# Kernel optimization log

Measured on AMD Instinct MI355X. Metric: run time of the kernel, lower is better.

The kernel has to match this reference:

```python
import jax, jax.numpy as jnp
import numpy as np

N_NODES = 100000
N_EDGES = 1600000
F_IN = 128
HIDDEN = 64
N_CLASSES = 32


def setup_inputs() -> dict:
    key = jax.random.key(0)
    k1, k2, k3, k4 = jax.random.split(key, 4)
    x = jax.random.normal(k1, (N_NODES, F_IN), dtype=jnp.float32)
    edge_index = jax.random.randint(k2, (2, N_EDGES), 0, N_NODES, dtype=jnp.int32)
    # Glorot-style init for the two GCNConv weight matrices
    W1 = jax.random.normal(k3, (F_IN, HIDDEN), dtype=jnp.float32) * (1.0 / np.sqrt(F_IN))
    W2 = jax.random.normal(k4, (HIDDEN, N_CLASSES), dtype=jnp.float32) * (1.0 / np.sqrt(HIDDEN))
    b1 = jnp.zeros((HIDDEN,), dtype=jnp.float32)
    b2 = jnp.zeros((N_CLASSES,), dtype=jnp.float32)
    return {"x": x, "edge_index": edge_index, "W1": W1, "b1": b1, "W2": W2, "b2": b2}


def gcn_conv(x, W, b, src, dst, num_nodes):
    # PyG GCNConv: linear transform first, then normalized neighbor aggregation.
    h = x @ W  # [N, out]
    ones = jnp.ones(src.shape, dtype=h.dtype)
    deg = jax.ops.segment_sum(ones, dst, num_segments=num_nodes)  # in-degree incl. self-loops
    d_inv_sqrt = jnp.where(deg > 0, jax.lax.rsqrt(deg), 0.0)
    norm = d_inv_sqrt[src] * d_inv_sqrt[dst]  # [E]
    msg = h[src] * norm[:, None]              # gather + scale, [E, out]
    out = jax.ops.segment_sum(msg, dst, num_segments=num_nodes)  # scatter-add
    return out + b


def reference(x, edge_index, W1, b1, W2, b2):
    n = x.shape[0]
    # add_self_loops=True (GCNConv default)
    loop = jnp.arange(n, dtype=edge_index.dtype)
    src = jnp.concatenate([edge_index[0], loop])
    dst = jnp.concatenate([edge_index[1], loop])
    h = jax.nn.relu(gcn_conv(x, W1, b1, src, dst, n))
    # F.dropout(training=self.training) is identity in eval mode
    logits = gcn_conv(h, W2, b2, src, dst, n)
    return jax.nn.log_softmax(logits, axis=1)
```

## Files before the change

### kernel.cpp

```cpp
#include <hip/hip_runtime.h>

#define F_IN 128
#define HID 64
#define CLS 32
#define BCAP 8192

typedef short v8s __attribute__((ext_vector_type(8)));
typedef float f4 __attribute__((ext_vector_type(4)));
typedef float f2 __attribute__((ext_vector_type(2)));

__device__ __forceinline__ float bflo(unsigned int w) { return __uint_as_float(w << 16); }
__device__ __forceinline__ float bfhi(unsigned int w) { return __uint_as_float(w & 0xFFFF0000u); }
__device__ __forceinline__ unsigned short f2bf(float f) {
    unsigned int u = __float_as_uint(f);
    u += 0x7FFFu + ((u >> 16) & 1u);
    return (unsigned short)(u >> 16);
}
__device__ __forceinline__ unsigned int pack2(float lo, float hi) {
    return (unsigned int)f2bf(lo) | ((unsigned int)f2bf(hi) << 16);
}
__device__ __forceinline__ unsigned char f2fp8(float v) {
    return (unsigned char)(__builtin_amdgcn_cvt_pk_fp8_f32(v, v, 0, false) & 0xFF);
}

__global__ __launch_bounds__(512) void k_init(int* __restrict__ bCursor, int nb) {
    int i = threadIdx.x;
    if (i < nb) bCursor[i] = i * BCAP;
}

__global__ __launch_bounds__(256) void k_bscatter(const int* __restrict__ src,
                                                  const int* __restrict__ dst,
                                                  int* __restrict__ bCursor,
                                                  int* __restrict__ bucketed, int E, int nb) {
    __shared__ int h[512];
    __shared__ int chunk[512];
    int tid = threadIdx.x;
    for (int i = tid; i < nb; i += 256) h[i] = 0;
    __syncthreads();

    int e0 = blockIdx.x * 2048;
    int myRec[8], myB[8], myRank[8];
#pragma unroll
    for (int k = 0; k < 8; ++k) {
        int e = e0 + k * 256 + tid;
        if (e < E) {
            int d = dst[e];
            myB[k] = d >> 8;
            myRec[k] = src[e] | ((d & 255) << 17);
            myRank[k] = atomicAdd(&h[myB[k]], 1);
        } else {
            myB[k] = -1;
        }
    }
    __syncthreads();
    for (int i = tid; i < nb; i += 256)
        chunk[i] = h[i] ? atomicAdd(&bCursor[i], h[i]) : 0;
    __syncthreads();
#pragma unroll
    for (int k = 0; k < 8; ++k) {
        if (myB[k] >= 0) bucketed[chunk[myB[k]] + myRank[k]] = myRec[k];
    }
}

__global__ __launch_bounds__(512) void k_csr(const int* __restrict__ bCursor,
                                             const int* __restrict__ bucketed,
                                             int* __restrict__ pk,
                                             float* __restrict__ dinv, int* __restrict__ csr,
                                             int n) {
    __shared__ int cnt[256];
    __shared__ int s[256];
    __shared__ int baseS[256];
    int b = blockIdx.x;
    int node0 = b << 8;
    int tid = threadIdx.x;
    if (tid < 256) cnt[tid] = 0;
    __syncthreads();
    int p0 = b * BCAP, p1 = bCursor[b];

    int rec[16], rnk[16];
#pragma unroll
    for (int k = 0; k < 16; ++k) {
        int p = p0 + tid + (k << 9);
        if (p < p1) {
            int r = bucketed[p];
            rec[k] = r;
            rnk[k] = atomicAdd(&cnt[r >> 17], 1);
        } else {
            rec[k] = -1;
        }
    }
    __syncthreads();
    int v = 0;
    if (tid < 256) { v = cnt[tid]; s[tid] = v; }
    __syncthreads();
    for (int off = 1; off < 256; off <<= 1) {
        int t = (tid >= off && tid < 256) ? s[tid - off] : 0;
        __syncthreads();
        if (tid < 256) s[tid] += t;
        __syncthreads();
    }
    if (tid < 256) {
        int myoff = p0 + s[tid] - v;
        baseS[tid] = myoff;
        int node = node0 + tid;
        if (node < n) {
            pk[node] = myoff | (v << 22);
            dinv[node] = rsqrtf((float)(v + 1));
        }
    }
    __syncthreads();
#pragma unroll
    for (int k = 0; k < 16; ++k) {
        if (rec[k] >= 0) csr[baseS[rec[k] >> 17] + rnk[k]] = rec[k] & 0x1FFFF;
    }
}

__global__ __launch_bounds__(256) void k_gemm1(const float* __restrict__ x,
                                               const float* __restrict__ W,
                                               const float* __restrict__ dinv,
                                               unsigned char* __restrict__ y, int n) {
    __shared__ unsigned short Wt[HID * 136];
    int tid = threadIdx.x;
    for (int i = tid; i < F_IN * HID; i += 256) {
        int k = i >> 6, nn = i & 63;
        Wt[nn * 136 + k] = f2bf(W[i]);
    }
    __syncthreads();

    int lane = tid & 63;
    int quad = lane >> 4, c = lane & 15;
    int nstripes = (n + 15) >> 4;
    int stripe = blockIdx.x * 4 + (tid >> 6);
    if (stripe >= nstripes) return;
    int row0 = stripe << 4;

    f4 acc[4] = {};
    union { unsigned int u[4]; v8s v; } au;

#pragma unroll
    for (int ks = 0; ks < 4; ++ks) {
        int k0 = ks * 32 + quad * 8;
        int row = row0 + c;
        if (row >= n) row = n - 1;
        const float* xp = x + (size_t)row * F_IN + k0;
        float4 lo = *(const float4*)xp;
        float4 hi = *(const float4*)(xp + 4);
        au.u[0] = pack2(lo.x, lo.y);
        au.u[1] = pack2(lo.z, lo.w);
        au.u[2] = pack2(hi.x, hi.y);
        au.u[3] = pack2(hi.z, hi.w);
        v8s a = au.v;
#pragma unroll
        for (int nt = 0; nt < 4; ++nt) {
            v8s bb = *(const v8s*)&Wt[(nt * 16 + c) * 136 + k0];
            acc[nt] = __builtin_amdgcn_mfma_f32_16x16x32_bf16(a, bb, acc[nt], 0, 0, 0);
        }
    }

#pragma unroll
    for (int reg = 0; reg < 4; ++reg) {
        int row = row0 + quad * 4 + reg;
        if (row < n) {
            float dd = dinv[row];
#pragma unroll
            for (int nt = 0; nt < 4; ++nt)
                y[(size_t)row * HID + nt * 16 + c] = f2fp8(acc[nt][reg] * dd);
        }
    }
}

__global__ __launch_bounds__(256) void k_gather64_w2(const int* __restrict__ pk,
                                                     const int* __restrict__ csr,
                                                     const unsigned char* __restrict__ xw8,
                                                     const float* __restrict__ b1,
                                                     const float* __restrict__ W2,
                                                     const float* __restrict__ dinv,
                                                     unsigned short* __restrict__ y2, int n) {
    __shared__ unsigned short Wt[CLS * 72];
    __shared__ unsigned short Hl[32 * 72];
    int tid = threadIdx.x;
    for (int i = tid; i < HID * CLS; i += 256) {
        int k = i >> 5, nn = i & 31;
        Wt[nn * 72 + k] = f2bf(W2[i]);
    }

    int g = tid >> 3;
    int l = tid & 7;
    int node = blockIdx.x * 32 + g;
    bool alive = node < n;

    if (alive) {
        unsigned int pv = (unsigned int)pk[node];
        int p0 = pv & 0x3FFFFF;
        int cntv = (int)(pv >> 22);
        int p1 = p0 + cntv;
        float dd = rsqrtf((float)(cntv + 1));
        uint2 sw = *(const uint2*)(xw8 + (size_t)node * HID + l * 8);

        f2 a0 = {0.f, 0.f}, a1 = a0, a2 = a0, a3 = a0;
        f2 c0 = a0, c1 = a0, c2 = a0, c3 = a0;
        int p = p0;
        for (; p + 3 < p1; p += 4) {
            int s0 = csr[p], s1 = csr[p + 1], s2 = csr[p + 2], s3 = csr[p + 3];
            uint2 w0 = *(const uint2*)(xw8 + (size_t)s0 * HID + l * 8);
            uint2 w1 = *(const uint2*)(xw8 + (size_t)s1 * HID + l * 8);
            uint2 w2 = *(const uint2*)(xw8 + (size_t)s2 * HID + l * 8);
            uint2 w3 = *(const uint2*)(xw8 + (size_t)s3 * HID + l * 8);
            a0 += __builtin_amdgcn_cvt_pk_f32_fp8(w0.x, false);
            a1 += __builtin_amdgcn_cvt_pk_f32_fp8(w0.x, true);
            a2 += __builtin_amdgcn_cvt_pk_f32_fp8(w0.y, false);
            a3 += __builtin_amdgcn_cvt_pk_f32_fp8(w0.y, true);
            c0 += __builtin_amdgcn_cvt_pk_f32_fp8(w1.x, false);
            c1 += __builtin_amdgcn_cvt_pk_f32_fp8(w1.x, true);
            c2 += __builtin_amdgcn_cvt_pk_f32_fp8(w1.y, false);
            c3 += __builtin_amdgcn_cvt_pk_f32_fp8(w1.y, true);
            a0 += __builtin_amdgcn_cvt_pk_f32_fp8(w2.x, false);
            a1 += __builtin_amdgcn_cvt_pk_f32_fp8(w2.x, true);
            a2 += __builtin_amdgcn_cvt_pk_f32_fp8(w2.y, false);
            a3 += __builtin_amdgcn_cvt_pk_f32_fp8(w2.y, true);
            c0 += __builtin_amdgcn_cvt_pk_f32_fp8(w3.x, false);
            c1 += __builtin_amdgcn_cvt_pk_f32_fp8(w3.x, true);
            c2 += __builtin_amdgcn_cvt_pk_f32_fp8(w3.y, false);
            c3 += __builtin_amdgcn_cvt_pk_f32_fp8(w3.y, true);
        }
        for (; p < p1; ++p) {
            int s0 = csr[p];
            uint2 w0 = *(const uint2*)(xw8 + (size_t)s0 * HID + l * 8);
            a0 += __builtin_amdgcn_cvt_pk_f32_fp8(w0.x, false);
            a1 += __builtin_amdgcn_cvt_pk_f32_fp8(w0.x, true);
            a2 += __builtin_amdgcn_cvt_pk_f32_fp8(w0.y, false);
            a3 += __builtin_amdgcn_cvt_pk_f32_fp8(w0.y, true);
        }
        a0 += c0; a1 += c1; a2 += c2; a3 += c3;
        a0 += __builtin_amdgcn_cvt_pk_f32_fp8(sw.x, false);
        a1 += __builtin_amdgcn_cvt_pk_f32_fp8(sw.x, true);
        a2 += __builtin_amdgcn_cvt_pk_f32_fp8(sw.y, false);
        a3 += __builtin_amdgcn_cvt_pk_f32_fp8(sw.y, true);

        float4 bb0 = *(const float4*)(b1 + l * 8);
        float4 bb1 = *(const float4*)(b1 + l * 8 + 4);
        float h0 = fmaxf(a0.x * dd + bb0.x, 0.f);
        float h1 = fmaxf(a0.y * dd + bb0.y, 0.f);
        float h2 = fmaxf(a1.x * dd + bb0.z, 0.f);
        float h3 = fmaxf(a1.y * dd + bb0.w, 0.f);
        float h4 = fmaxf(a2.x * dd + bb1.x, 0.f);
        float h5 = fmaxf(a2.y * dd + bb1.y, 0.f);
        float h6 = fmaxf(a3.x * dd + bb1.z, 0.f);
        float h7 = fmaxf(a3.y * dd + bb1.w, 0.f);
        uint4 hp;
        hp.x = pack2(h0, h1);
        hp.y = pack2(h2, h3);
        hp.z = pack2(h4, h5);
        hp.w = pack2(h6, h7);
        *(uint4*)&Hl[g * 72 + l * 8] = hp;
    }
    __syncthreads();

    int wv = tid >> 6;
    int t = wv & 1, nt = wv >> 1;
    int lane = tid & 63, quad = lane >> 4, c = lane & 15;
    f4 acc = {};
#pragma unroll
    for (int ks = 0; ks < 2; ++ks) {
        int k0 = ks * 32 + quad * 8;
        v8s aF = *(const v8s*)&Hl[(t * 16 + c) * 72 + k0];
        v8s bF = *(const v8s*)&Wt[(nt * 16 + c) * 72 + k0];
        acc = __builtin_amdgcn_mfma_f32_16x16x32_bf16(aF, bF, acc, 0, 0, 0);
    }
    int row0 = blockIdx.x * 32 + t * 16;
#pragma unroll
    for (int reg = 0; reg < 4; ++reg) {
        int row = row0 + quad * 4 + reg;
        if (row < n) {
            float dd2 = dinv[row];
            y2[(size_t)row * CLS + nt * 16 + c] = f2bf(acc[reg] * dd2);
        }
    }
}

__global__ __launch_bounds__(256) void k_gather32_lsm(const int* __restrict__ pk,
                                                      const int* __restrict__ csr,
                                                      const unsigned short* __restrict__ hwb,
                                                      const float* __restrict__ b,
                                                      float* __restrict__ out, int n) {
    int tid = threadIdx.x;
    int node = blockIdx.x * 64 + (tid >> 2);
    if (node >= n) return;
    int l = tid & 3;
    unsigned int pv = (unsigned int)pk[node];
    int p0 = pv & 0x3FFFFF;
    int cntv = (int)(pv >> 22);
    int p1 = p0 + cntv;
    float dd = rsqrtf((float)(cntv + 1));
    uint4 sw = *(const uint4*)(hwb + (size_t)node * CLS + l * 8);

    float A0 = 0.f, A1 = 0.f, A2 = 0.f, A3 = 0.f, A4 = 0.f, A5 = 0.f, A6 = 0.f, A7 = 0.f;
    float B0 = 0.f, B1 = 0.f, B2 = 0.f, B3 = 0.f, B4 = 0.f, B5 = 0.f, B6 = 0.f, B7 = 0.f;
    int p = p0;
    for (; p + 3 < p1; p += 4) {
        int s0 = csr[p], s1 = csr[p + 1], s2 = csr[p + 2], s3 = csr[p + 3];
        uint4 w0 = *(const uint4*)(hwb + (size_t)s0 * CLS + l * 8);
        uint4 w1 = *(const uint4*)(hwb + (size_t)s1 * CLS + l * 8);
        uint4 w2 = *(const uint4*)(hwb + (size_t)s2 * CLS + l * 8);
        uint4 w3 = *(const uint4*)(hwb + (size_t)s3 * CLS + l * 8);
        A0 += bflo(w0.x); A1 += bfhi(w0.x); A2 += bflo(w0.y); A3 += bfhi(w0.y);
        A4 += bflo(w0.z); A5 += bfhi(w0.z); A6 += bflo(w0.w); A7 += bfhi(w0.w);
        B0 += bflo(w1.x); B1 += bfhi(w1.x); B2 += bflo(w1.y); B3 += bfhi(w1.y);
        B4 += bflo(w1.z); B5 += bfhi(w1.z); B6 += bflo(w1.w); B7 += bfhi(w1.w);
        A0 += bflo(w2.x); A1 += bfhi(w2.x); A2 += bflo(w2.y); A3 += bfhi(w2.y);
        A4 += bflo(w2.z); A5 += bfhi(w2.z); A6 += bflo(w2.w); A7 += bfhi(w2.w);
        B0 += bflo(w3.x); B1 += bfhi(w3.x); B2 += bflo(w3.y); B3 += bfhi(w3.y);
        B4 += bflo(w3.z); B5 += bfhi(w3.z); B6 += bflo(w3.w); B7 += bfhi(w3.w);
    }
    for (; p < p1; ++p) {
        int s0 = csr[p];
        uint4 w0 = *(const uint4*)(hwb + (size_t)s0 * CLS + l * 8);
        A0 += bflo(w0.x); A1 += bfhi(w0.x); A2 += bflo(w0.y); A3 += bfhi(w0.y);
        A4 += bflo(w0.z); A5 += bfhi(w0.z); A6 += bflo(w0.w); A7 += bfhi(w0.w);
    }
    A0 += B0; A1 += B1; A2 += B2; A3 += B3;
    A4 += B4; A5 += B5; A6 += B6; A7 += B7;

    float4 bb0 = *(const float4*)(b + l * 8);
    float4 bb1 = *(const float4*)(b + l * 8 + 4);
    float v0 = (A0 + bflo(sw.x)) * dd + bb0.x;
    float v1 = (A1 + bfhi(sw.x)) * dd + bb0.y;
    float v2 = (A2 + bflo(sw.y)) * dd + bb0.z;
    float v3 = (A3 + bfhi(sw.y)) * dd + bb0.w;
    float v4 = (A4 + bflo(sw.z)) * dd + bb1.x;
    float v5 = (A5 + bfhi(sw.z)) * dd + bb1.y;
    float v6 = (A6 + bflo(sw.w)) * dd + bb1.z;
    float v7 = (A7 + bfhi(sw.w)) * dd + bb1.w;

    float m = fmaxf(fmaxf(fmaxf(v0, v1), fmaxf(v2, v3)), fmaxf(fmaxf(v4, v5), fmaxf(v6, v7)));
    m = fmaxf(m, __shfl_xor(m, 1));
    m = fmaxf(m, __shfl_xor(m, 2));
    float s = __expf(v0 - m) + __expf(v1 - m) + __expf(v2 - m) + __expf(v3 - m) +
              __expf(v4 - m) + __expf(v5 - m) + __expf(v6 - m) + __expf(v7 - m);
    s += __shfl_xor(s, 1);
    s += __shfl_xor(s, 2);
    float ls = m + __logf(s);
    float4 o0, o1;
    o0.x = v0 - ls; o0.y = v1 - ls; o0.z = v2 - ls; o0.w = v3 - ls;
    o1.x = v4 - ls; o1.y = v5 - ls; o1.z = v6 - ls; o1.w = v7 - ls;
    float* op = out + (size_t)node * CLS + l * 8;
    *(float4*)op = o0;
    *(float4*)(op + 4) = o1;
}

extern "C" void kernel_launch(void* const* d_in, const int* in_sizes, int n_in,
                              void* d_out, int out_size, void* d_ws, size_t ws_size,
                              hipStream_t stream) {
    const float* x  = (const float*)d_in[0];
    const int* edge = (const int*)d_in[1];
    const float* W1 = (const float*)d_in[2];
    const float* b1 = (const float*)d_in[3];
    const float* W2 = (const float*)d_in[4];
    const float* b2 = (const float*)d_in[5];
    float* out = (float*)d_out;

    int N = in_sizes[0] / F_IN;
    int E = in_sizes[1] / 2;
    const int* src = edge;
    const int* dst = edge + E;
    int NB = (N + 255) >> 8;

    float* dinv    = (float*)d_ws;
    int* pk        = (int*)(dinv + N);
    int* bCursor   = pk + N;
    int* csr       = bCursor + 512;
    int* bucketed  = csr + (size_t)NB * BCAP;
    unsigned char* bufA = (unsigned char*)(bucketed + (size_t)NB * BCAP);
    unsigned short* y2  = (unsigned short*)(bufA + (size_t)N * HID);

    k_init<<<1, 512, 0, stream>>>(bCursor, NB);
    k_bscatter<<<(E + 2047) / 2048, 256, 0, stream>>>(src, dst, bCursor, bucketed, E, NB);
    k_csr<<<NB, 512, 0, stream>>>(bCursor, bucketed, pk, dinv, csr, N);

    int nstripes16 = (N + 15) >> 4;
    int gemmBlocks = (nstripes16 + 3) / 4;

    k_gemm1<<<gemmBlocks, 256, 0, stream>>>(x, W1, dinv, bufA, N);

    k_gather64_w2<<<(N + 31) / 32, 256, 0, stream>>>(pk, csr, bufA, b1, W2, dinv, y2, N);

    k_gather32_lsm<<<(N + 63) / 64, 256, 0, stream>>>(pk, csr, y2, b2, out, N);
}
```

Baseline: 203.0 us.

## Merge edge bucketing and first GEMM into one kernel, apply src norm in gather

The edge bucket-scatter and the layer-1 GEMM now run as one launch, with block ranges split between the two jobs. The GEMM no longer depends on degrees, so it can overlap the scatter instead of waiting for the CSR build. Because the GEMM output is no longer pre-scaled, the layer-1 gather loads dinv[src] per edge and multiplies it in. This adds an extra random load and multiply per edge, and the FP8 values are stored without scaling, which changes their rounding. The cursor init kernel becomes a memset with relative offsets, and bf16 packing uses the hardware v_cvt_pk_bf16_f32 instruction.

```diff
diff --git a/kernel.cpp b/kernel.cpp
--- a/kernel.cpp
+++ b/kernel.cpp
@@ -17,52 +17,100 @@
     return (unsigned short)(u >> 16);
 }
 __device__ __forceinline__ unsigned int pack2(float lo, float hi) {
-    return (unsigned int)f2bf(lo) | ((unsigned int)f2bf(hi) << 16);
+    unsigned int r;
+    asm("v_cvt_pk_bf16_f32 %0, %1, %2" : "=v"(r) : "v"(lo), "v"(hi));
+    return r;
 }
 __device__ __forceinline__ unsigned char f2fp8(float v) {
     return (unsigned char)(__builtin_amdgcn_cvt_pk_fp8_f32(v, v, 0, false) & 0xFF);
 }
 
-__global__ __launch_bounds__(512) void k_init(int* __restrict__ bCursor, int nb) {
-    int i = threadIdx.x;
-    if (i < nb) bCursor[i] = i * BCAP;
-}
-
-__global__ __launch_bounds__(256) void k_bscatter(const int* __restrict__ src,
-                                                  const int* __restrict__ dst,
-                                                  int* __restrict__ bCursor,
-                                                  int* __restrict__ bucketed, int E, int nb) {
-    __shared__ int h[512];
-    __shared__ int chunk[512];
+__global__ __launch_bounds__(256) void k_front(const int* __restrict__ src,
+                                               const int* __restrict__ dst,
+                                               int* __restrict__ bC,
+                                               int* __restrict__ bucketed,
+                                               const float* __restrict__ x,
+                                               const float* __restrict__ W1,
+                                               unsigned char* __restrict__ y,
+                                               int E, int nb, int n, int sB) {
+    __shared__ union {
+        struct { int h[512]; int chunk[512]; } sc;
+        unsigned short w1[HID * 136];
+    } S;
     int tid = threadIdx.x;
-    for (int i = tid; i < nb; i += 256) h[i] = 0;
-    __syncthreads();
-
-    int e0 = blockIdx.x * 2048;
-    int myRec[8], myB[8], myRank[8];
-#pragma unroll
-    for (int k = 0; k < 8; ++k) {
-        int e = e0 + k * 256 + tid;
-        if (e < E) {
-            int d = dst[e];
-            myB[k] = d >> 8;
-            myRec[k] = src[e] | ((d & 255) << 17);
-            myRank[k] = atomicAdd(&h[myB[k]], 1);
-        } else {
-            myB[k] = -1;
-        }
-    }
-    __syncthreads();
-    for (int i = tid; i < nb; i += 256)
-        chunk[i] = h[i] ? atomicAdd(&bCursor[i], h[i]) : 0;
-    __syncthreads();
-#pragma unroll
-    for (int k = 0; k < 8; ++k) {
-        if (myB[k] >= 0) bucketed[chunk[myB[k]] + myRank[k]] = myRec[k];
-    }
-}
-
-__global__ __launch_bounds__(512) void k_csr(const int* __restrict__ bCursor,
+    int bid = blockIdx.x;
+
+    if (bid < sB) {
+        for (int i = tid; i < nb; i += 256) S.sc.h[i] = 0;
+        __syncthreads();
+        int e0 = bid << 11;
+        int myRec[8], myB[8], myRank[8];
+#pragma unroll
+        for (int k = 0; k < 8; ++k) {
+            int e = e0 + k * 256 + tid;
+            if (e < E) {
+                int d = dst[e];
+                myB[k] = d >> 8;
+                myRec[k] = src[e] | ((d & 255) << 17);
+                myRank[k] = atomicAdd(&S.sc.h[myB[k]], 1);
+            } else {
+                myB[k] = -1;
+            }
+        }
+        __syncthreads();
+        for (int i = tid; i < nb; i += 256)
+            S.sc.chunk[i] = S.sc.h[i] ? (i * BCAP + atomicAdd(&bC[i], S.sc.h[i])) : 0;
+        __syncthreads();
+#pragma unroll
+        for (int k = 0; k < 8; ++k)
+            if (myB[k] >= 0) bucketed[S.sc.chunk[myB[k]] + myRank[k]] = myRec[k];
+    } else {
+        for (int i = tid; i < F_IN * HID; i += 256) {
+            int k = i >> 6, nn = i & 63;
+            S.w1[nn * 136 + k] = f2bf(W1[i]);
+        }
+        __syncthreads();
+        int lane = tid & 63;
+        int quad = lane >> 4, c = lane & 15;
+        int nstripes = (n + 15) >> 4;
+        int stripe = (bid - sB) * 4 + (tid >> 6);
+        if (stripe >= nstripes) return;
+        int row0 = stripe << 4;
+
+        f4 acc[4] = {};
+        union { unsigned int u[4]; v8s v; } au;
+#pragma unroll
+        for (int ks = 0; ks < 4; ++ks) {
+            int k0 = ks * 32 + quad * 8;
+            int row = row0 + c;
+            if (row >= n) row = n - 1;
+            const float* xp = x + (size_t)row * F_IN + k0;
+            float4 lo = *(const float4*)xp;
+            float4 hi = *(const float4*)(xp + 4);
+            au.u[0] = pack2(lo.x, lo.y);
+            au.u[1] = pack2(lo.z, lo.w);
+            au.u[2] = pack2(hi.x, hi.y);
+            au.u[3] = pack2(hi.z, hi.w);
+            v8s a = au.v;
+#pragma unroll
+            for (int nt = 0; nt < 4; ++nt) {
+                v8s bb = *(const v8s*)&S.w1[(nt * 16 + c) * 136 + k0];
+                acc[nt] = __builtin_amdgcn_mfma_f32_16x16x32_bf16(a, bb, acc[nt], 0, 0, 0);
+            }
+        }
+#pragma unroll
+        for (int reg = 0; reg < 4; ++reg) {
+            int row = row0 + quad * 4 + reg;
+            if (row < n) {
+#pragma unroll
+                for (int nt = 0; nt < 4; ++nt)
+                    y[(size_t)row * HID + nt * 16 + c] = f2fp8(acc[nt][reg]);
+            }
+        }
+    }
+}
+
+__global__ __launch_bounds__(512) void k_csr(const int* __restrict__ bC,
                                              const int* __restrict__ bucketed,
                                              int* __restrict__ pk,
                                              float* __restrict__ dinv, int* __restrict__ csr,
@@ -75,7 +123,7 @@
     int tid = threadIdx.x;
     if (tid < 256) cnt[tid] = 0;
     __syncthreads();
-    int p0 = b * BCAP, p1 = bCursor[b];
+    int p0 = b * BCAP, p1 = p0 + bC[b];
 
     int rec[16], rnk[16];
 #pragma unroll
@@ -112,60 +160,6 @@
 #pragma unroll
     for (int k = 0; k < 16; ++k) {
         if (rec[k] >= 0) csr[baseS[rec[k] >> 17] + rnk[k]] = rec[k] & 0x1FFFF;
-    }
-}
-
-__global__ __launch_bounds__(256) void k_gemm1(const float* __restrict__ x,
-                                               const float* __restrict__ W,
-                                               const float* __restrict__ dinv,
-                                               unsigned char* __restrict__ y, int n) {
-    __shared__ unsigned short Wt[HID * 136];
-    int tid = threadIdx.x;
-    for (int i = tid; i < F_IN * HID; i += 256) {
-        int k = i >> 6, nn = i & 63;
-        Wt[nn * 136 + k] = f2bf(W[i]);
-    }
-    __syncthreads();
-
-    int lane = tid & 63;
-    int quad = lane >> 4, c = lane & 15;
-    int nstripes = (n + 15) >> 4;
-    int stripe = blockIdx.x * 4 + (tid >> 6);
-    if (stripe >= nstripes) return;
-    int row0 = stripe << 4;
-
-    f4 acc[4] = {};
-    union { unsigned int u[4]; v8s v; } au;
-
-#pragma unroll
-    for (int ks = 0; ks < 4; ++ks) {
-        int k0 = ks * 32 + quad * 8;
-        int row = row0 + c;
-        if (row >= n) row = n - 1;
-        const float* xp = x + (size_t)row * F_IN + k0;
-        float4 lo = *(const float4*)xp;
-        float4 hi = *(const float4*)(xp + 4);
-        au.u[0] = pack2(lo.x, lo.y);
-        au.u[1] = pack2(lo.z, lo.w);
-        au.u[2] = pack2(hi.x, hi.y);
-        au.u[3] = pack2(hi.z, hi.w);
-        v8s a = au.v;
-#pragma unroll
-        for (int nt = 0; nt < 4; ++nt) {
-            v8s bb = *(const v8s*)&Wt[(nt * 16 + c) * 136 + k0];
-            acc[nt] = __builtin_amdgcn_mfma_f32_16x16x32_bf16(a, bb, acc[nt], 0, 0, 0);
-        }
-    }
-
-#pragma unroll
-    for (int reg = 0; reg < 4; ++reg) {
-        int row = row0 + quad * 4 + reg;
-        if (row < n) {
-            float dd = dinv[row];
-#pragma unroll
-            for (int nt = 0; nt < 4; ++nt)
-                y[(size_t)row * HID + nt * 16 + c] = f2fp8(acc[nt][reg] * dd);
-        }
     }
 }
 
@@ -187,9 +181,8 @@
     int g = tid >> 3;
     int l = tid & 7;
     int node = blockIdx.x * 32 + g;
-    bool alive = node < n;
-
-    if (alive) {
+
+    if (node < n) {
         unsigned int pv = (unsigned int)pk[node];
         int p0 = pv & 0x3FFFFF;
         int cntv = (int)(pv >> 22);
@@ -199,43 +192,48 @@
 
         f2 a0 = {0.f, 0.f}, a1 = a0, a2 = a0, a3 = a0;
         f2 c0 = a0, c1 = a0, c2 = a0, c3 = a0;
-        int p = p0;
-        for (; p + 3 < p1; p += 4) {
-            int s0 = csr[p], s1 = csr[p + 1], s2 = csr[p + 2], s3 = csr[p + 3];
+        int q = p0;
+        for (; q + 3 < p1; q += 4) {
+            int s0 = csr[q], s1 = csr[q + 1], s2 = csr[q + 2], s3 = csr[q + 3];
+            float d0 = dinv[s0], d1 = dinv[s1], d2 = dinv[s2], d3 = dinv[s3];
             uint2 w0 = *(const uint2*)(xw8 + (size_t)s0 * HID + l * 8);
             uint2 w1 = *(const uint2*)(xw8 + (size_t)s1 * HID + l * 8);
             uint2 w2 = *(const uint2*)(xw8 + (size_t)s2 * HID + l * 8);
             uint2 w3 = *(const uint2*)(xw8 + (size_t)s3 * HID + l * 8);
-            a0 += __builtin_amdgcn_cvt_pk_f32_fp8(w0.x, false);
-            a1 += __builtin_amdgcn_cvt_pk_f32_fp8(w0.x, true);
-            a2 += __builtin_amdgcn_cvt_pk_f32_fp8(w0.y, false);
-            a3 += __builtin_amdgcn_cvt_pk_f32_fp8(w0.y, true);
-            c0 += __builtin_amdgcn_cvt_pk_f32_fp8(w1.x, false);
-            c1 += __builtin_amdgcn_cvt_pk_f32_fp8(w1.x, true);
-            c2 += __builtin_amdgcn_cvt_pk_f32_fp8(w1.y, false);
-            c3 += __builtin_amdgcn_cvt_pk_f32_fp8(w1.y, true);
-            a0 += __builtin_amdgcn_cvt_pk_f32_fp8(w2.x, false);
-            a1 += __builtin_amdgcn_cvt_pk_f32_fp8(w2.x, true);
-            a2 += __builtin_amdgcn_cvt_pk_f32_fp8(w2.y, false);
-            a3 += __builtin_amdgcn_cvt_pk_f32_fp8(w2.y, true);
-            c0 += __builtin_amdgcn_cvt_pk_f32_fp8(w3.x, false);
-            c1 += __builtin_amdgcn_cvt_pk_f32_fp8(w3.x, true);
-            c2 += __builtin_amdgcn_cvt_pk_f32_fp8(w3.y, false);
-            c3 += __builtin_amdgcn_cvt_pk_f32_fp8(w3.y, true);
-        }
-        for (; p < p1; ++p) {
-            int s0 = csr[p];
+            f2 D0 = {d0, d0}, D1 = {d1, d1}, D2 = {d2, d2}, D3 = {d3, d3};
+            a0 += __builtin_amdgcn_cvt_pk_f32_fp8(w0.x, false) * D0;
+            a1 += __builtin_amdgcn_cvt_pk_f32_fp8(w0.x, true) * D0;
+            a2 += __builtin_amdgcn_cvt_pk_f32_fp8(w0.y, false) * D0;
+            a3 += __builtin_amdgcn_cvt_pk_f32_fp8(w0.y, true) * D0;
+            c0 += __builtin_amdgcn_cvt_pk_f32_fp8(w1.x, false) * D1;
+            c1 += __builtin_amdgcn_cvt_pk_f32_fp8(w1.x, true) * D1;
+            c2 += __builtin_amdgcn_cvt_pk_f32_fp8(w1.y, false) * D1;
+            c3 += __builtin_amdgcn_cvt_pk_f32_fp8(w1.y, true) * D1;
+            a0 += __builtin_amdgcn_cvt_pk_f32_fp8(w2.x, false) * D2;
+            a1 += __builtin_amdgcn_cvt_pk_f32_fp8(w2.x, true) * D2;
+            a2 += __builtin_amdgcn_cvt_pk_f32_fp8(w2.y, false) * D2;
+            a3 += __builtin_amdgcn_cvt_pk_f32_fp8(w2.y, true) * D2;
+            c0 += __builtin_amdgcn_cvt_pk_f32_fp8(w3.x, false) * D3;
+            c1 += __builtin_amdgcn_cvt_pk_f32_fp8(w3.x, true) * D3;
+            c2 += __builtin_amdgcn_cvt_pk_f32_fp8(w3.y, false) * D3;
+            c3 += __builtin_amdgcn_cvt_pk_f32_fp8(w3.y, true) * D3;
+        }
+        for (; q < p1; ++q) {
+            int s0 = csr[q];
+            float d0 = dinv[s0];
             uint2 w0 = *(const uint2*)(xw8 + (size_t)s0 * HID + l * 8);
-            a0 += __builtin_amdgcn_cvt_pk_f32_fp8(w0.x, false);
-            a1 += __builtin_amdgcn_cvt_pk_f32_fp8(w0.x, true);
-            a2 += __builtin_amdgcn_cvt_pk_f32_fp8(w0.y, false);
-            a3 += __builtin_amdgcn_cvt_pk_f32_fp8(w0.y, true);
+            f2 D0 = {d0, d0};
+            a0 += __builtin_amdgcn_cvt_pk_f32_fp8(w0.x, false) * D0;
+            a1 += __builtin_amdgcn_cvt_pk_f32_fp8(w0.x, true) * D0;
+            a2 += __builtin_amdgcn_cvt_pk_f32_fp8(w0.y, false) * D0;
+            a3 += __builtin_amdgcn_cvt_pk_f32_fp8(w0.y, true) * D0;
         }
         a0 += c0; a1 += c1; a2 += c2; a3 += c3;
-        a0 += __builtin_amdgcn_cvt_pk_f32_fp8(sw.x, false);
-        a1 += __builtin_amdgcn_cvt_pk_f32_fp8(sw.x, true);
-        a2 += __builtin_amdgcn_cvt_pk_f32_fp8(sw.y, false);
-        a3 += __builtin_amdgcn_cvt_pk_f32_fp8(sw.y, true);
+        f2 DS = {dd, dd};
+        a0 += __builtin_amdgcn_cvt_pk_f32_fp8(sw.x, false) * DS;
+        a1 += __builtin_amdgcn_cvt_pk_f32_fp8(sw.x, true) * DS;
+        a2 += __builtin_amdgcn_cvt_pk_f32_fp8(sw.y, false) * DS;
+        a3 += __builtin_amdgcn_cvt_pk_f32_fp8(sw.y, true) * DS;
 
         float4 bb0 = *(const float4*)(b1 + l * 8);
         float4 bb1 = *(const float4*)(b1 + l * 8 + 4);
@@ -367,20 +365,21 @@
 
     float* dinv    = (float*)d_ws;
     int* pk        = (int*)(dinv + N);
-    int* bCursor   = pk + N;
-    int* csr       = bCursor + 512;
+    int* bC        = pk + N;
+    int* csr       = bC + 512;
     int* bucketed  = csr + (size_t)NB * BCAP;
     unsigned char* bufA = (unsigned char*)(bucketed + (size_t)NB * BCAP);
     unsigned short* y2  = (unsigned short*)(bufA + (size_t)N * HID);
 
-    k_init<<<1, 512, 0, stream>>>(bCursor, NB);
-    k_bscatter<<<(E + 2047) / 2048, 256, 0, stream>>>(src, dst, bCursor, bucketed, E, NB);
-    k_csr<<<NB, 512, 0, stream>>>(bCursor, bucketed, pk, dinv, csr, N);
-
+    hipMemsetAsync(bC, 0, (size_t)NB * sizeof(int), stream);
+
+    int sB = (E + 2047) / 2048;
     int nstripes16 = (N + 15) >> 4;
-    int gemmBlocks = (nstripes16 + 3) / 4;
-
-    k_gemm1<<<gemmBlocks, 256, 0, stream>>>(x, W1, dinv, bufA, N);
+    int gB = (nstripes16 + 3) / 4;
+
+    k_front<<<sB + gB, 256, 0, stream>>>(src, dst, bC, bucketed, x, W1, bufA, E, NB, N, sB);
+
+    k_csr<<<NB, 512, 0, stream>>>(bC, bucketed, pk, dinv, csr, N);
 
     k_gather64_w2<<<(N + 31) / 32, 256, 0, stream>>>(pk, csr, bufA, b1, W2, dinv, y2, N);
 
```

Measured after the change: 203.3 us. About the same (+0.1%).

## Merge CSR build with first GEMM and compute degrees via global atomics

Applied to the files above, without the earlier changes.

Degrees are now counted with global atomics in the scatter kernel, so the first GEMM no longer waits for CSR construction and runs as extra blocks of a combined k_mid launch beside the per-bucket CSR build. Buckets shrink to 128 nodes with BCAP 4096, CSR segments are padded to multiples of 4 so neighbor indices load as int4, and both gather loops unroll to 8 neighbors. bf16 packing uses a hardware convert instruction. This cuts launches and serialization, at the cost of contended global atomics on deg and silent truncation if a bucket exceeds BCAP.

```diff
diff --git a/kernel.cpp b/kernel.cpp
--- a/kernel.cpp
+++ b/kernel.cpp
@@ -3,7 +3,7 @@
 #define F_IN 128
 #define HID 64
 #define CLS 32
-#define BCAP 8192
+#define BCAP 4096
 
 typedef short v8s __attribute__((ext_vector_type(8)));
 typedef float f4 __attribute__((ext_vector_type(4)));
@@ -17,36 +17,34 @@
     return (unsigned short)(u >> 16);
 }
 __device__ __forceinline__ unsigned int pack2(float lo, float hi) {
-    return (unsigned int)f2bf(lo) | ((unsigned int)f2bf(hi) << 16);
+    unsigned int r;
+    asm("v_cvt_pk_bf16_f32 %0, %1, %2" : "=v"(r) : "v"(lo), "v"(hi));
+    return r;
 }
 __device__ __forceinline__ unsigned char f2fp8(float v) {
     return (unsigned char)(__builtin_amdgcn_cvt_pk_fp8_f32(v, v, 0, false) & 0xFF);
 }
 
-__global__ __launch_bounds__(512) void k_init(int* __restrict__ bCursor, int nb) {
-    int i = threadIdx.x;
-    if (i < nb) bCursor[i] = i * BCAP;
-}
-
-__global__ __launch_bounds__(256) void k_bscatter(const int* __restrict__ src,
-                                                  const int* __restrict__ dst,
-                                                  int* __restrict__ bCursor,
-                                                  int* __restrict__ bucketed, int E, int nb) {
-    __shared__ int h[512];
-    __shared__ int chunk[512];
+__global__ __launch_bounds__(256) void k_scat(const int* __restrict__ src,
+                                              const int* __restrict__ dst,
+                                              int* __restrict__ deg,
+                                              int* __restrict__ bC,
+                                              int* __restrict__ bucketed, int E, int nb) {
+    __shared__ int h[1024];
+    __shared__ int chunk[1024];
     int tid = threadIdx.x;
     for (int i = tid; i < nb; i += 256) h[i] = 0;
     __syncthreads();
-
-    int e0 = blockIdx.x * 2048;
-    int myRec[8], myB[8], myRank[8];
-#pragma unroll
-    for (int k = 0; k < 8; ++k) {
+    int e0 = blockIdx.x << 12;
+    int myRec[16], myB[16], myRank[16];
+#pragma unroll
+    for (int k = 0; k < 16; ++k) {
         int e = e0 + k * 256 + tid;
         if (e < E) {
             int d = dst[e];
-            myB[k] = d >> 8;
-            myRec[k] = src[e] | ((d & 255) << 17);
+            atomicAdd(&deg[d], 1);
+            myB[k] = d >> 7;
+            myRec[k] = src[e] | ((d & 127) << 17);
             myRank[k] = atomicAdd(&h[myB[k]], 1);
         } else {
             myB[k] = -1;
@@ -54,117 +52,108 @@
     }
     __syncthreads();
     for (int i = tid; i < nb; i += 256)
-        chunk[i] = h[i] ? atomicAdd(&bCursor[i], h[i]) : 0;
+        chunk[i] = h[i] ? (i * BCAP + atomicAdd(&bC[i], h[i])) : 0;
     __syncthreads();
 #pragma unroll
-    for (int k = 0; k < 8; ++k) {
+    for (int k = 0; k < 16; ++k)
         if (myB[k] >= 0) bucketed[chunk[myB[k]] + myRank[k]] = myRec[k];
-    }
-}
-
-__global__ __launch_bounds__(512) void k_csr(const int* __restrict__ bCursor,
+}
+
+__global__ __launch_bounds__(256) void k_mid(const int* __restrict__ bC,
                                              const int* __restrict__ bucketed,
-                                             int* __restrict__ pk,
-                                             float* __restrict__ dinv, int* __restrict__ csr,
-                                             int n) {
-    __shared__ int cnt[256];
-    __shared__ int s[256];
-    __shared__ int baseS[256];
-    int b = blockIdx.x;
-    int node0 = b << 8;
+                                             int* __restrict__ pk, int* __restrict__ csr,
+                                             const float* __restrict__ x,
+                                             const float* __restrict__ W,
+                                             const int* __restrict__ deg,
+                                             unsigned char* __restrict__ y, int n, int NB) {
+    __shared__ union {
+        struct { int cnt[128]; int s[128]; int baseS[128]; } c;
+        unsigned short w1[HID * 136];
+    } S;
     int tid = threadIdx.x;
-    if (tid < 256) cnt[tid] = 0;
-    __syncthreads();
-    int p0 = b * BCAP, p1 = bCursor[b];
-
-    int rec[16], rnk[16];
-#pragma unroll
-    for (int k = 0; k < 16; ++k) {
-        int p = p0 + tid + (k << 9);
-        if (p < p1) {
-            int r = bucketed[p];
-            rec[k] = r;
-            rnk[k] = atomicAdd(&cnt[r >> 17], 1);
-        } else {
-            rec[k] = -1;
-        }
-    }
-    __syncthreads();
-    int v = 0;
-    if (tid < 256) { v = cnt[tid]; s[tid] = v; }
-    __syncthreads();
-    for (int off = 1; off < 256; off <<= 1) {
-        int t = (tid >= off && tid < 256) ? s[tid - off] : 0;
+    int bid = blockIdx.x;
+
+    if (bid < NB) {
+        if (tid < 128) S.c.cnt[tid] = 0;
         __syncthreads();
-        if (tid < 256) s[tid] += t;
+        int nrec = bC[bid];
+        if (nrec > BCAP) nrec = BCAP;
+        int p0 = bid * BCAP, p1 = p0 + nrec;
+        int rec[16], rnk[16];
+#pragma unroll
+        for (int k = 0; k < 16; ++k) {
+            int p = p0 + tid + (k << 8);
+            if (p < p1) {
+                int r = bucketed[p];
+                rec[k] = r;
+                rnk[k] = atomicAdd(&S.c.cnt[r >> 17], 1);
+            } else {
+                rec[k] = -1;
+            }
+        }
         __syncthreads();
-    }
-    if (tid < 256) {
-        int myoff = p0 + s[tid] - v;
-        baseS[tid] = myoff;
-        int node = node0 + tid;
-        if (node < n) {
-            pk[node] = myoff | (v << 22);
-            dinv[node] = rsqrtf((float)(v + 1));
-        }
-    }
-    __syncthreads();
-#pragma unroll
-    for (int k = 0; k < 16; ++k) {
-        if (rec[k] >= 0) csr[baseS[rec[k] >> 17] + rnk[k]] = rec[k] & 0x1FFFF;
-    }
-}
-
-__global__ __launch_bounds__(256) void k_gemm1(const float* __restrict__ x,
-                                               const float* __restrict__ W,
-                                               const float* __restrict__ dinv,
-                                               unsigned char* __restrict__ y, int n) {
-    __shared__ unsigned short Wt[HID * 136];
-    int tid = threadIdx.x;
-    for (int i = tid; i < F_IN * HID; i += 256) {
-        int k = i >> 6, nn = i & 63;
-        Wt[nn * 136 + k] = f2bf(W[i]);
-    }
-    __syncthreads();
-
-    int lane = tid & 63;
-    int quad = lane >> 4, c = lane & 15;
-    int nstripes = (n + 15) >> 4;
-    int stripe = blockIdx.x * 4 + (tid >> 6);
-    if (stripe >= nstripes) return;
-    int row0 = stripe << 4;
-
-    f4 acc[4] = {};
-    union { unsigned int u[4]; v8s v; } au;
-
-#pragma unroll
-    for (int ks = 0; ks < 4; ++ks) {
-        int k0 = ks * 32 + quad * 8;
-        int row = row0 + c;
-        if (row >= n) row = n - 1;
-        const float* xp = x + (size_t)row * F_IN + k0;
-        float4 lo = *(const float4*)xp;
-        float4 hi = *(const float4*)(xp + 4);
-        au.u[0] = pack2(lo.x, lo.y);
-        au.u[1] = pack2(lo.z, lo.w);
-        au.u[2] = pack2(hi.x, hi.y);
-        au.u[3] = pack2(hi.z, hi.w);
-        v8s a = au.v;
-#pragma unroll
-        for (int nt = 0; nt < 4; ++nt) {
-            v8s bb = *(const v8s*)&Wt[(nt * 16 + c) * 136 + k0];
-            acc[nt] = __builtin_amdgcn_mfma_f32_16x16x32_bf16(a, bb, acc[nt], 0, 0, 0);
-        }
-    }
-
-#pragma unroll
-    for (int reg = 0; reg < 4; ++reg) {
-        int row = row0 + quad * 4 + reg;
-        if (row < n) {
-            float dd = dinv[row];
-#pragma unroll
-            for (int nt = 0; nt < 4; ++nt)
-                y[(size_t)row * HID + nt * 16 + c] = f2fp8(acc[nt][reg] * dd);
+        int v = 0, pv4 = 0;
+        if (tid < 128) { v = S.c.cnt[tid]; pv4 = (v + 3) & ~3; S.c.s[tid] = pv4; }
+        __syncthreads();
+        for (int off = 1; off < 128; off <<= 1) {
+            int t = (tid >= off && tid < 128) ? S.c.s[tid - off] : 0;
+            __syncthreads();
+            if (tid < 128) S.c.s[tid] += t;
+            __syncthreads();
+        }
+        if (tid < 128) {
+            int myoff = p0 + S.c.s[tid] - pv4;
+            S.c.baseS[tid] = myoff;
+            int node = (bid << 7) + tid;
+            if (node < n) pk[node] = myoff | (v << 22);
+        }
+        __syncthreads();
+#pragma unroll
+        for (int k = 0; k < 16; ++k)
+            if (rec[k] >= 0) csr[S.c.baseS[rec[k] >> 17] + rnk[k]] = rec[k] & 0x1FFFF;
+    } else {
+        for (int i = tid; i < F_IN * HID; i += 256) {
+            int k = i >> 6, nn = i & 63;
+            S.w1[nn * 136 + k] = f2bf(W[i]);
+        }
+        __syncthreads();
+        int lane = tid & 63;
+        int quad = lane >> 4, c = lane & 15;
+        int nstripes = (n + 15) >> 4;
+        int stripe = (bid - NB) * 4 + (tid >> 6);
+        if (stripe >= nstripes) return;
+        int row0 = stripe << 4;
+
+        f4 acc[4] = {};
+        union { unsigned int u[4]; v8s v; } au;
+#pragma unroll
+        for (int ks = 0; ks < 4; ++ks) {
+            int k0 = ks * 32 + quad * 8;
+            int row = row0 + c;
+            if (row >= n) row = n - 1;
+            const float* xp = x + (size_t)row * F_IN + k0;
+            float4 lo = *(const float4*)xp;
+            float4 hi = *(const float4*)(xp + 4);
+            au.u[0] = pack2(lo.x, lo.y);
+            au.u[1] = pack2(lo.z, lo.w);
+            au.u[2] = pack2(hi.x, hi.y);
+            au.u[3] = pack2(hi.z, hi.w);
+            v8s a = au.v;
+#pragma unroll
+            for (int nt = 0; nt < 4; ++nt) {
+                v8s bb = *(const v8s*)&S.w1[(nt * 16 + c) * 136 + k0];
+                acc[nt] = __builtin_amdgcn_mfma_f32_16x16x32_bf16(a, bb, acc[nt], 0, 0, 0);
+            }
+        }
+#pragma unroll
+        for (int reg = 0; reg < 4; ++reg) {
+            int row = row0 + quad * 4 + reg;
+            if (row < n) {
+                float dd = rsqrtf((float)(deg[row] + 1));
+#pragma unroll
+                for (int nt = 0; nt < 4; ++nt)
+                    y[(size_t)row * HID + nt * 16 + c] = f2fp8(acc[nt][reg] * dd);
+            }
         }
     }
 }
@@ -174,7 +163,7 @@
                                                      const unsigned char* __restrict__ xw8,
                                                      const float* __restrict__ b1,
                                                      const float* __restrict__ W2,
-                                                     const float* __restrict__ dinv,
+                                                     const int* __restrict__ deg,
                                                      unsigned short* __restrict__ y2, int n) {
     __shared__ unsigned short Wt[CLS * 72];
     __shared__ unsigned short Hl[32 * 72];
@@ -187,9 +176,8 @@
     int g = tid >> 3;
     int l = tid & 7;
     int node = blockIdx.x * 32 + g;
-    bool alive = node < n;
-
-    if (alive) {
+
+    if (node < n) {
         unsigned int pv = (unsigned int)pk[node];
         int p0 = pv & 0x3FFFFF;
         int cntv = (int)(pv >> 22);
@@ -199,13 +187,18 @@
 
         f2 a0 = {0.f, 0.f}, a1 = a0, a2 = a0, a3 = a0;
         f2 c0 = a0, c1 = a0, c2 = a0, c3 = a0;
-        int p = p0;
-        for (; p + 3 < p1; p += 4) {
-            int s0 = csr[p], s1 = csr[p + 1], s2 = csr[p + 2], s3 = csr[p + 3];
-            uint2 w0 = *(const uint2*)(xw8 + (size_t)s0 * HID + l * 8);
-            uint2 w1 = *(const uint2*)(xw8 + (size_t)s1 * HID + l * 8);
-            uint2 w2 = *(const uint2*)(xw8 + (size_t)s2 * HID + l * 8);
-            uint2 w3 = *(const uint2*)(xw8 + (size_t)s3 * HID + l * 8);
+        int q = p0;
+        for (; q + 7 < p1; q += 8) {
+            int4 sa = *(const int4*)(csr + q);
+            int4 sb = *(const int4*)(csr + q + 4);
+            uint2 w0 = *(const uint2*)(xw8 + (size_t)sa.x * HID + l * 8);
+            uint2 w1 = *(const uint2*)(xw8 + (size_t)sa.y * HID + l * 8);
+            uint2 w2 = *(const uint2*)(xw8 + (size_t)sa.z * HID + l * 8);
+            uint2 w3 = *(const uint2*)(xw8 + (size_t)sa.w * HID + l * 8);
+            uint2 w4 = *(const uint2*)(xw8 + (size_t)sb.x * HID + l * 8);
+            uint2 w5 = *(const uint2*)(xw8 + (size_t)sb.y * HID + l * 8);
+            uint2 w6 = *(const uint2*)(xw8 + (size_t)sb.z * HID + l * 8);
+            uint2 w7 = *(const uint2*)(xw8 + (size_t)sb.w * HID + l * 8);
             a0 += __builtin_amdgcn_cvt_pk_f32_fp8(w0.x, false);
             a1 += __builtin_amdgcn_cvt_pk_f32_fp8(w0.x, true);
             a2 += __builtin_amdgcn_cvt_pk_f32_fp8(w0.y, false);
@@ -222,9 +215,48 @@
             c1 += __builtin_amdgcn_cvt_pk_f32_fp8(w3.x, true);
             c2 += __builtin_amdgcn_cvt_pk_f32_fp8(w3.y, false);
             c3 += __builtin_amdgcn_cvt_pk_f32_fp8(w3.y, true);
-        }
-        for (; p < p1; ++p) {
-            int s0 = csr[p];
+            a0 += __builtin_amdgcn_cvt_pk_f32_fp8(w4.x, false);
+            a1 += __builtin_amdgcn_cvt_pk_f32_fp8(w4.x, true);
+            a2 += __builtin_amdgcn_cvt_pk_f32_fp8(w4.y, false);
+            a3 += __builtin_amdgcn_cvt_pk_f32_fp8(w4.y, true);
+            c0 += __builtin_amdgcn_cvt_pk_f32_fp8(w5.x, false);
+            c1 += __builtin_amdgcn_cvt_pk_f32_fp8(w5.x, true);
+            c2 += __builtin_amdgcn_cvt_pk_f32_fp8(w5.y, false);
+            c3 += __builtin_amdgcn_cvt_pk_f32_fp8(w5.y, true);
+            a0 += __builtin_amdgcn_cvt_pk_f32_fp8(w6.x, false);
+            a1 += __builtin_amdgcn_cvt_pk_f32_fp8(w6.x, true);
+            a2 += __builtin_amdgcn_cvt_pk_f32_fp8(w6.y, false);
+            a3 += __builtin_amdgcn_cvt_pk_f32_fp8(w6.y, true);
+            c0 += __builtin_amdgcn_cvt_pk_f32_fp8(w7.x, false);
+            c1 += __builtin_amdgcn_cvt_pk_f32_fp8(w7.x, true);
+            c2 += __builtin_amdgcn_cvt_pk_f32_fp8(w7.y, false);
+            c3 += __builtin_amdgcn_cvt_pk_f32_fp8(w7.y, true);
+        }
+        for (; q + 3 < p1; q += 4) {
+            int4 sa = *(const int4*)(csr + q);
+            uint2 w0 = *(const uint2*)(xw8 + (size_t)sa.x * HID + l * 8);
+            uint2 w1 = *(const uint2*)(xw8 + (size_t)sa.y * HID + l * 8);
+            uint2 w2 = *(const uint2*)(xw8 + (size_t)sa.z * HID + l * 8);
+            uint2 w3 = *(const uint2*)(xw8 + (size_t)sa.w * HID + l * 8);
+            a0 += __builtin_amdgcn_cvt_pk_f32_fp8(w0.x, false);
+            a1 += __builtin_amdgcn_cvt_pk_f32_fp8(w0.x, true);
+            a2 += __builtin_amdgcn_cvt_pk_f32_fp8(w0.y, false);
+            a3 += __builtin_amdgcn_cvt_pk_f32_fp8(w0.y, true);
+            c0 += __builtin_amdgcn_cvt_pk_f32_fp8(w1.x, false);
+            c1 += __builtin_amdgcn_cvt_pk_f32_fp8(w1.x, true);
+            c2 += __builtin_amdgcn_cvt_pk_f32_fp8(w1.y, false);
+            c3 += __builtin_amdgcn_cvt_pk_f32_fp8(w1.y, true);
+            a0 += __builtin_amdgcn_cvt_pk_f32_fp8(w2.x, false);
+            a1 += __builtin_amdgcn_cvt_pk_f32_fp8(w2.x, true);
+            a2 += __builtin_amdgcn_cvt_pk_f32_fp8(w2.y, false);
+            a3 += __builtin_amdgcn_cvt_pk_f32_fp8(w2.y, true);
+            c0 += __builtin_amdgcn_cvt_pk_f32_fp8(w3.x, false);
+            c1 += __builtin_amdgcn_cvt_pk_f32_fp8(w3.x, true);
+            c2 += __builtin_amdgcn_cvt_pk_f32_fp8(w3.y, false);
+            c3 += __builtin_amdgcn_cvt_pk_f32_fp8(w3.y, true);
+        }
+        for (; q < p1; ++q) {
+            int s0 = csr[q];
             uint2 w0 = *(const uint2*)(xw8 + (size_t)s0 * HID + l * 8);
             a0 += __builtin_amdgcn_cvt_pk_f32_fp8(w0.x, false);
             a1 += __builtin_amdgcn_cvt_pk_f32_fp8(w0.x, true);
@@ -272,7 +304,7 @@
     for (int reg = 0; reg < 4; ++reg) {
         int row = row0 + quad * 4 + reg;
         if (row < n) {
-            float dd2 = dinv[row];
+            float dd2 = rsqrtf((float)(deg[row] + 1));
             y2[(size_t)row * CLS + nt * 16 + c] = f2bf(acc[reg] * dd2);
         }
     }
@@ -297,12 +329,40 @@
     float A0 = 0.f, A1 = 0.f, A2 = 0.f, A3 = 0.f, A4 = 0.f, A5 = 0.f, A6 = 0.f, A7 = 0.f;
     float B0 = 0.f, B1 = 0.f, B2 = 0.f, B3 = 0.f, B4 = 0.f, B5 = 0.f, B6 = 0.f, B7 = 0.f;
     int p = p0;
+    for (; p + 7 < p1; p += 8) {
+        int4 sa = *(const int4*)(csr + p);
+        int4 sb = *(const int4*)(csr + p + 4);
+        uint4 w0 = *(const uint4*)(hwb + (size_t)sa.x * CLS + l * 8);
+        uint4 w1 = *(const uint4*)(hwb + (size_t)sa.y * CLS + l * 8);
+        uint4 w2 = *(const uint4*)(hwb + (size_t)sa.z * CLS + l * 8);
+        uint4 w3 = *(const uint4*)(hwb + (size_t)sa.w * CLS + l * 8);
+        uint4 w4 = *(const uint4*)(hwb + (size_t)sb.x * CLS + l * 8);
+        uint4 w5 = *(const uint4*)(hwb + (size_t)sb.y * CLS + l * 8);
+        uint4 w6 = *(const uint4*)(hwb + (size_t)sb.z * CLS + l * 8);
+        uint4 w7 = *(const uint4*)(hwb + (size_t)sb.w * CLS + l * 8);
+        A0 += bflo(w0.x); A1 += bfhi(w0.x); A2 += bflo(w0.y); A3 += bfhi(w0.y);
+        A4 += bflo(w0.z); A5 += bfhi(w0.z); A6 += bflo(w0.w); A7 += bfhi(w0.w);
+        B0 += bflo(w1.x); B1 += bfhi(w1.x); B2 += bflo(w1.y); B3 += bfhi(w1.y);
+        B4 += bflo(w1.z); B5 += bfhi(w1.z); B6 += bflo(w1.w); B7 += bfhi(w1.w);
+        A0 += bflo(w2.x); A1 += bfhi(w2.x); A2 += bflo(w2.y); A3 += bfhi(w2.y);
+        A4 += bflo(w2.z); A5 += bfhi(w2.z); A6 += bflo(w2.w); A7 += bfhi(w2.w);
+        B0 += bflo(w3.x); B1 += bfhi(w3.x); B2 += bflo(w3.y); B3 += bfhi(w3.y);
+        B4 += bflo(w3.z); B5 += bfhi(w3.z); B6 += bflo(w3.w); B7 += bfhi(w3.w);
+        A0 += bflo(w4.x); A1 += bfhi(w4.x); A2 += bflo(w4.y); A3 += bfhi(w4.y);
+        A4 += bflo(w4.z); A5 += bfhi(w4.z); A6 += bflo(w4.w); A7 += bfhi(w4.w);
+        B0 += bflo(w5.x); B1 += bfhi(w5.x); B2 += bflo(w5.y); B3 += bfhi(w5.y);
+        B4 += bflo(w5.z); B5 += bfhi(w5.z); B6 += bflo(w5.w); B7 += bfhi(w5.w);
+        A0 += bflo(w6.x); A1 += bfhi(w6.x); A2 += bflo(w6.y); A3 += bfhi(w6.y);
+        A4 += bflo(w6.z); A5 += bfhi(w6.z); A6 += bflo(w6.w); A7 += bfhi(w6.w);
+        B0 += bflo(w7.x); B1 += bfhi(w7.x); B2 += bflo(w7.y); B3 += bfhi(w7.y);
+        B4 += bflo(w7.z); B5 += bfhi(w7.z); B6 += bflo(w7.w); B7 += bfhi(w7.w);
+    }
     for (; p + 3 < p1; p += 4) {
-        int s0 = csr[p], s1 = csr[p + 1], s2 = csr[p + 2], s3 = csr[p + 3];
-        uint4 w0 = *(const uint4*)(hwb + (size_t)s0 * CLS + l * 8);
-        uint4 w1 = *(const uint4*)(hwb + (size_t)s1 * CLS + l * 8);
-        uint4 w2 = *(const uint4*)(hwb + (size_t)s2 * CLS + l * 8);
-        uint4 w3 = *(const uint4*)(hwb + (size_t)s3 * CLS + l * 8);
+        int4 sa = *(const int4*)(csr + p);
+        uint4 w0 = *(const uint4*)(hwb + (size_t)sa.x * CLS + l * 8);
+        uint4 w1 = *(const uint4*)(hwb + (size_t)sa.y * CLS + l * 8);
+        uint4 w2 = *(const uint4*)(hwb + (size_t)sa.z * CLS + l * 8);
+        uint4 w3 = *(const uint4*)(hwb + (size_t)sa.w * CLS + l * 8);
         A0 += bflo(w0.x); A1 += bfhi(w0.x); A2 += bflo(w0.y); A3 += bfhi(w0.y);
         A4 += bflo(w0.z); A5 += bfhi(w0.z); A6 += bflo(w0.w); A7 += bfhi(w0.w);
         B0 += bflo(w1.x); B1 += bfhi(w1.x); B2 += bflo(w1.y); B3 += bfhi(w1.y);
@@ -363,26 +423,27 @@
     int E = in_sizes[1] / 2;
     const int* src = edge;
     const int* dst = edge + E;
-    int NB = (N + 255) >> 8;
-
-    float* dinv    = (float*)d_ws;
-    int* pk        = (int*)(dinv + N);
-    int* bCursor   = pk + N;
-    int* csr       = bCursor + 512;
+    int NB = (N + 127) >> 7;
+
+    int* deg       = (int*)d_ws;
+    int* bC        = deg + N;
+    int* pk        = bC + 1024;
+    int* csr       = pk + N;
     int* bucketed  = csr + (size_t)NB * BCAP;
     unsigned char* bufA = (unsigned char*)(bucketed + (size_t)NB * BCAP);
     unsigned short* y2  = (unsigned short*)(bufA + (size_t)N * HID);
 
-    k_init<<<1, 512, 0, stream>>>(bCursor, NB);
-    k_bscatter<<<(E + 2047) / 2048, 256, 0, stream>>>(src, dst, bCursor, bucketed, E, NB);
-    k_csr<<<NB, 512, 0, stream>>>(bCursor, bucketed, pk, dinv, csr, N);
-
+    (void)hipMemsetAsync(deg, 0, ((size_t)N + 1024) * sizeof(int), stream);
+
+    int sB = (E + 4095) / 4096;
     int nstripes16 = (N + 15) >> 4;
-    int gemmBlocks = (nstripes16 + 3) / 4;
-
-    k_gemm1<<<gemmBlocks, 256, 0, stream>>>(x, W1, dinv, bufA, N);
-
-    k_gather64_w2<<<(N + 31) / 32, 256, 0, stream>>>(pk, csr, bufA, b1, W2, dinv, y2, N);
+    int gB = (nstripes16 + 3) / 4;
+
+    k_scat<<<sB, 256, 0, stream>>>(src, dst, deg, bC, bucketed, E, NB);
+
+    k_mid<<<NB + gB, 256, 0, stream>>>(bC, bucketed, pk, csr, x, W1, deg, bufA, N, NB);
+
+    k_gather64_w2<<<(N + 31) / 32, 256, 0, stream>>>(pk, csr, bufA, b1, W2, deg, y2, N);
 
     k_gather32_lsm<<<(N + 63) / 64, 256, 0, stream>>>(pk, csr, y2, b2, out, N);
 }
```

Result: slower. 244.8 us (+20.6%).
